# Kernel optimization log

Measured on AMD Instinct MI355X. Metric: run time of the kernel, lower is better.

The kernel has to match this reference:

```python
import jax, jax.numpy as jnp
import numpy as np

NUM_USERS = 100000
NUM_ITEMS = 50000
NUM_EDGES = 1000000
H = 64            # initial embedding dim
DIMS = [64, 64]   # per-layer output dims
B = 16384         # BPR batch size
NEG_SLOPE = 0.2
EPS = 1e-12


def setup_inputs() -> dict:
    key = jax.random.key(0)
    ks = jax.random.split(key, 20)
    s = 1.0 / np.sqrt(H)
    inp = {
        'user_emb': jax.random.normal(ks[0], (NUM_USERS, H), jnp.float32) * 0.1,
        'item_emb': jax.random.normal(ks[1], (NUM_ITEMS, H), jnp.float32) * 0.1,
        'W1_0': jax.random.normal(ks[2], (H, DIMS[0]), jnp.float32) * s,
        'b1_0': jnp.zeros((DIMS[0],), jnp.float32),
        'W2_0': jax.random.normal(ks[3], (H, DIMS[0]), jnp.float32) * s,
        'b2_0': jnp.zeros((DIMS[0],), jnp.float32),
        'W1_1': jax.random.normal(ks[4], (DIMS[0], DIMS[1]), jnp.float32) * s,
        'b1_1': jnp.zeros((DIMS[1],), jnp.float32),
        'W2_1': jax.random.normal(ks[5], (DIMS[0], DIMS[1]), jnp.float32) * s,
        'b2_1': jnp.zeros((DIMS[1],), jnp.float32),
        'edge_index': jnp.stack([
            jax.random.randint(ks[6], (NUM_EDGES,), 0, NUM_USERS),
            jax.random.randint(ks[7], (NUM_EDGES,), 0, NUM_ITEMS),
        ], axis=0),
        'users': jax.random.randint(ks[8], (B,), 0, NUM_USERS),
        'pos_items': jax.random.randint(ks[9], (B,), 0, NUM_ITEMS),
        'neg_items': jax.random.randint(ks[10], (B,), 0, NUM_ITEMS),
    }
    return inp


def _edge_norm(src, dst):
    # symmetric sqrt-degree norm: (deg_src * deg_dst) ** -0.5 per edge
    ones = jnp.ones(src.shape[0], jnp.float32)
    du = jax.ops.segment_sum(ones, src, num_segments=NUM_USERS)[src]
    di = jax.ops.segment_sum(ones, dst, num_segments=NUM_ITEMS)[dst]
    return ((du * di) ** -0.5)[:, None]  # [E, 1]


def _epilogue(h):
    # leaky_relu(0.2) -> (dropout eval = identity) -> L2 row-normalize
    h = jnp.where(h >= 0, h, NEG_SLOPE * h)
    n = jnp.sqrt(jnp.sum(h * h, axis=1, keepdims=True))
    return h / jnp.maximum(n, EPS)


def _layer(u, i, src, dst, norm, W1, b1, W2, b2):
    # node-level W1 transform, gathered per edge (same math as per-edge W1(x_j))
    u1 = u @ W1 + b1            # [Nu, d]
    i1 = i @ W1 + b1            # [Ni, d]
    cross = u[src] * i[dst]     # [E, din]  shared by both directions
    mW2 = cross @ W2 + b2       # [E, d]
    # user -> item: x_j = user[src], aggregate at item dst
    out_i = jax.ops.segment_sum(norm * u1[src] + mW2, dst, num_segments=NUM_ITEMS)
    # item -> user: x_j = item[dst], aggregate at user src
    out_u = jax.ops.segment_sum(norm * i1[dst] + mW2, src, num_segments=NUM_USERS)
    return _epilogue(out_u), _epilogue(out_i)


def reference(user_emb, item_emb, W1_0, b1_0, W2_0, b2_0, W1_1, b1_1, W2_1, b2_1,
              edge_index, users, pos_items, neg_items):
    src, dst = edge_index[0], edge_index[1]
    norm = _edge_norm(src, dst)
    u_list, i_list = [user_emb], [item_emb]
    u, i = user_emb, item_emb
    u, i = _layer(u, i, src, dst, norm, W1_0, b1_0, W2_0, b2_0)
    u_list.append(u); i_list.append(i)
    u, i = _layer(u, i, src, dst, norm, W1_1, b1_1, W2_1, b2_1)
    u_list.append(u); i_list.append(i)
    user_all = jnp.concatenate(u_list, axis=1)   # [Nu, H+sum(DIMS)]
    item_all = jnp.concatenate(i_list, axis=1)   # [Ni, H+sum(DIMS)]
    return (user_all[users], item_all[pos_items], item_all[neg_items])
```

## Files before the change

### kernel.cpp

```cpp
#include <hip/hip_runtime.h>

#define NU 100000
#define NI 50000
#define NE 1000000
#define NB 16384

#define UB ((NU + 1023) / 1024)
#define IB ((NI + 1023) / 1024)

#define NBKT_I ((NI + 127) >> 7)
#define NBKT_U ((NU + 255) >> 8)
#define EPB 2048

__global__ void deg_kernel(const int* __restrict__ ei, int* du, int* di) {
    int e = blockIdx.x * blockDim.x + threadIdx.x;
    if (e >= NE) return;
    atomicAdd(&du[ei[e]], 1);
    atomicAdd(&di[ei[NE + e]], 1);
}

__global__ __launch_bounds__(1024) void scan1_kernel(
        const int* __restrict__ du, const int* __restrict__ di,
        int* __restrict__ psum, float* __restrict__ rsd_u, float* __restrict__ rsd_i) {
    int b = blockIdx.x, tid = threadIdx.x;
    int v = 0;
    if (b < UB) {
        int i = b * 1024 + tid;
        if (i < NU) {
            int d = du[i]; v = d;
            rsd_u[i] = d > 0 ? 1.0f / sqrtf((float)d) : 0.f;
        }
    } else {
        int i = (b - UB) * 1024 + tid;
        if (i < NI) {
            int d = di[i]; v = d;
            rsd_i[i] = d > 0 ? 1.0f / sqrtf((float)d) : 0.f;
        }
    }
    int s = v;
    #pragma unroll
    for (int off = 32; off > 0; off >>= 1) s += __shfl_xor(s, off);
    __shared__ int ws[16];
    if ((tid & 63) == 0) ws[tid >> 6] = s;
    __syncthreads();
    if (tid == 0) {
        int t = 0;
        #pragma unroll
        for (int w = 0; w < 16; ++w) t += ws[w];
        psum[b] = t;
    }
}

__global__ __launch_bounds__(128) void scan2_kernel(int* __restrict__ psum) {
    int base = (blockIdx.x == 0) ? 0 : UB;
    int n = (blockIdx.x == 0) ? UB : IB;
    int tid = threadIdx.x;
    __shared__ int sh[128];
    int v = (tid < n) ? psum[base + tid] : 0;
    sh[tid] = v;
    __syncthreads();
    for (int off = 1; off < 128; off <<= 1) {
        int t = (tid >= off) ? sh[tid - off] : 0;
        __syncthreads();
        sh[tid] += t;
        __syncthreads();
    }
    if (tid < n) psum[base + tid] = sh[tid] - v;
}

__global__ __launch_bounds__(1024) void scan3_kernel(
        const int* __restrict__ du, const int* __restrict__ di,
        const int* __restrict__ psum,
        int* __restrict__ rp_u, int* __restrict__ rp_i,
        int* __restrict__ bcur_u, int* __restrict__ bcur_i) {
    int b = blockIdx.x, tid = threadIdx.x;
    bool isU = (b < UB);
    const int* deg = isU ? du : di;
    int* rp = isU ? rp_u : rp_i;
    int N = isU ? NU : NI;
    int i0 = isU ? b * 1024 : (b - UB) * 1024;
    int i = i0 + tid;
    int v = (i < N) ? deg[i] : 0;
    __shared__ int sh[1024];
    sh[tid] = v;
    __syncthreads();
    for (int off = 1; off < 1024; off <<= 1) {
        int t = (tid >= off) ? sh[tid - off] : 0;
        __syncthreads();
        sh[tid] += t;
        __syncthreads();
    }
    int excl = sh[tid] - v + psum[b];
    if (i < N) {
        rp[i] = excl;
        if (isU) { if ((i & 255) == 0) bcur_u[i >> 8] = excl; }
        else     { if ((i & 127) == 0) bcur_i[i >> 7] = excl; }
    }
    if (b == 0 && tid == 0) { rp_u[NU] = NE; rp_i[NI] = NE; }
}

__global__ __launch_bounds__(256) void binP1_kernel(
        const int* __restrict__ ei,
        int* __restrict__ bcur_i, int* __restrict__ bcur_u,
        int2* __restrict__ pairI, int2* __restrict__ pairU) {
    __shared__ int histA[NBKT_I], baseA[NBKT_I];
    __shared__ int histB[NBKT_U], baseB[NBKT_U];
    int t = threadIdx.x;
    int e0 = blockIdx.x * EPB;
    int cnt = min(EPB, NE - e0);
    int s[8], d[8];
    #pragma unroll
    for (int k = 0; k < 8; ++k) {
        int o = t + k * 256;
        if (o < cnt) { s[k] = ei[e0 + o]; d[k] = ei[NE + e0 + o]; }
        else { s[k] = -1; d[k] = -1; }
    }
    for (int x = t; x < NBKT_I; x += 256) histA[x] = 0;
    for (int x = t; x < NBKT_U; x += 256) histB[x] = 0;
    __syncthreads();
    #pragma unroll
    for (int k = 0; k < 8; ++k) {
        if (d[k] >= 0) {
            atomicAdd(&histA[d[k] >> 7], 1);
            atomicAdd(&histB[s[k] >> 8], 1);
        }
    }
    __syncthreads();
    for (int x = t; x < NBKT_I; x += 256) {
        int h = histA[x];
        baseA[x] = h ? atomicAdd(&bcur_i[x], h) : 0;
        histA[x] = 0;
    }
    for (int x = t; x < NBKT_U; x += 256) {
        int h = histB[x];
        baseB[x] = h ? atomicAdd(&bcur_u[x], h) : 0;
        histB[x] = 0;
    }
    __syncthreads();
    #pragma unroll
    for (int k = 0; k < 8; ++k) {
        if (d[k] >= 0) {
            int bI = d[k] >> 7;
            int off = atomicAdd(&histA[bI], 1);
            pairI[baseA[bI] + off] = make_int2(d[k], s[k]);
            int bU = s[k] >> 8;
            int off2 = atomicAdd(&histB[bU], 1);
            pairU[baseB[bU] + off2] = make_int2(s[k], d[k]);
        }
    }
}

__global__ __launch_bounds__(256) void binP2_kernel(
        const int2* __restrict__ pairI, const int2* __restrict__ pairU,
        const int* __restrict__ rp_i, const int* __restrict__ rp_u,
        const float* __restrict__ rsd_u, const float* __restrict__ rsd_i,
        int2* __restrict__ csr8_i, int2* __restrict__ csr8_u) {
    __shared__ int cur[256];
    int t = threadIdx.x;
    if (blockIdx.x < NBKT_I) {
        int b = blockIdx.x;
        int nb = b << 7, ne = min(nb + 128, NI);
        if (t < ne - nb) cur[t] = rp_i[nb + t];
        int wbeg = rp_i[nb], wend = rp_i[ne];
        __syncthreads();
        for (int j = wbeg + t; j < wend; j += 256) {
            int2 p = pairI[j];
            int slot = atomicAdd(&cur[p.x - nb], 1);
            csr8_i[slot] = make_int2(p.y, __float_as_int(rsd_u[p.y]));
        }
    } else {
        int b = blockIdx.x - NBKT_I;
        int nb = b << 8, ne = min(nb + 256, NU);
        if (t < ne - nb) cur[t] = rp_u[nb + t];
        int wbeg = rp_u[nb], wend = rp_u[ne];
        __syncthreads();
        for (int j = wbeg + t; j < wend; j += 256) {
            int2 p = pairU[j];
            int slot = atomicAdd(&cur[p.x - nb], 1);
            csr8_u[slot] = make_int2(p.y, __float_as_int(rsd_i[p.y]));
        }
    }
}

__global__ __launch_bounds__(256) void gatherA_kernel(
        const float* __restrict__ xu, const float* __restrict__ xi,
        const int* __restrict__ rp_u, const int* __restrict__ rp_i,
        const int2* __restrict__ csr8_u, const int2* __restrict__ csr8_i,
        const float* __restrict__ rsd_u, const float* __restrict__ rsd_i,
        float* __restrict__ acbuf_u, float* __restrict__ acbuf_i,
        float* __restrict__ swbuf_u, float* __restrict__ swbuf_i) {
    int n = (blockIdx.x * blockDim.x + threadIdx.x) >> 6;
    int lane = threadIdx.x & 63;
    if (n >= NI + NU) return;
    bool isItem = n < NI;
    int nn = isItem ? n : n - NI;
    const int* rp = isItem ? rp_i : rp_u;
    const int2* cs = isItem ? csr8_i : csr8_u;
    const float* x_own = isItem ? xi : xu;
    const float* emb_o = isItem ? xu : xi;
    float rs = isItem ? rsd_i[nn] : rsd_u[nn];
    float* acbuf = isItem ? acbuf_i : acbuf_u;
    float* swbuf = isItem ? swbuf_i : swbuf_u;

    int beg = rp[nn], end = rp[nn + 1];
    float sp = 0.f, ss = 0.f, swp = 0.f;
    for (int jj = beg; jj < end; jj += 64) {
        int m = min(64, end - jj);
        int2 rec = (lane < m) ? cs[jj + lane] : make_int2(0, 0);
        int idx = rec.x;
        float w = __int_as_float(rec.y);
        swp += w;
        int t = 0;
        for (; t + 3 < m; t += 4) {
            int s0 = __shfl(idx, t),     s1 = __shfl(idx, t + 1);
            int s2 = __shfl(idx, t + 2), s3 = __shfl(idx, t + 3);
            float w0 = __shfl(w, t),     w1 = __shfl(w, t + 1);
            float w2 = __shfl(w, t + 2), w3 = __shfl(w, t + 3);
            float v0 = emb_o[(size_t)s0 * 64 + lane];
            float v1 = emb_o[(size_t)s1 * 64 + lane];
            float v2 = emb_o[(size_t)s2 * 64 + lane];
            float v3 = emb_o[(size_t)s3 * 64 + lane];
            sp += (v0 + v1) + (v2 + v3);
            ss += w0 * v0 + w1 * v1 + w2 * v2 + w3 * v3;
        }
        for (; t < m; ++t) {
            int s0 = __shfl(idx, t);
            float w0 = __shfl(w, t);
            float v0 = emb_o[(size_t)s0 * 64 + lane];
            sp += v0; ss += w0 * v0;
        }
    }
    #pragma unroll
    for (int off = 32; off > 0; off >>= 1) swp += __shfl_xor(swp, off);
    acbuf[(size_t)nn * 128 + lane] = rs * ss;
    acbuf[(size_t)nn * 128 + 64 + lane] = x_own[(size_t)nn * 64 + lane] * sp;
    if (lane == 0) swbuf[nn] = rs * swp;
}

#define TB 4
__global__ __launch_bounds__(256) void transformB_kernel(
        int N, const float* __restrict__ acbuf, const float* __restrict__ swbuf,
        const int* __restrict__ rp,
        const float* __restrict__ W1, const float* __restrict__ b1,
        const float* __restrict__ W2, const float* __restrict__ b2,
        float* __restrict__ out) {
    __shared__ float w1s[4096];
    __shared__ float w2s[4096];
    __shared__ float acs[4][TB * 128];
    int tid = threadIdx.x;
    #pragma unroll
    for (int r = 0; r < 4; ++r) {
        *(float4*)&w1s[(r * 256 + tid) * 4] = *(const float4*)&W1[(r * 256 + tid) * 4];
        *(float4*)&w2s[(r * 256 + tid) * 4] = *(const float4*)&W2[(r * 256 + tid) * 4];
    }
    __syncthreads();
    int wv = tid >> 6, lane = tid & 63;
    int n0 = (blockIdx.x * 4 + wv) * TB;
    if (n0 >= N) return;
    float* slab = acs[wv];
    int half = lane >> 5;
    int off = (lane & 31) * 4;
    #pragma unroll
    for (int pr = 0; pr < 2; ++pr) {
        int j = pr * 2 + half;
        int n = n0 + j; if (n >= N) n = N - 1;
        *(float4*)&slab[j * 128 + off] = *(const float4*)&acbuf[(size_t)n * 128 + off];
    }
    float acc[TB] = {0.f, 0.f, 0.f, 0.f};
    #pragma unroll 4
    for (int kq = 0; kq < 16; ++kq) {
        float4 aq[TB], cq[TB];
        #pragma unroll
        for (int j = 0; j < TB; ++j) {
            aq[j] = *(const float4*)&slab[j * 128 + kq * 4];
            cq[j] = *(const float4*)&slab[j * 128 + 64 + kq * 4];
        }
        #pragma unroll
        for (int kk = 0; kk < 4; ++kk) {
            int k = kq * 4 + kk;
            float w1v = w1s[k * 64 + lane];
            float w2v = w2s[k * 64 + lane];
            #pragma unroll
            for (int j = 0; j < TB; ++j)
                acc[j] += (&aq[j].x)[kk] * w1v + (&cq[j].x)[kk] * w2v;
        }
    }
    float b1v = b1[lane], b2v = b2[lane];
    #pragma unroll
    for (int j = 0; j < TB; ++j) {
        int n = n0 + j;
        if (n >= N) break;
        float dgf = (float)(rp[n + 1] - rp[n]);
        float h = acc[j] + swbuf[n] * b1v + dgf * b2v;
        h = h >= 0.f ? h : 0.2f * h;
        float nsq = h * h;
        #pragma unroll
        for (int o = 32; o > 0; o >>= 1) nsq += __shfl_xor(nsq, o);
        float nrm = sqrtf(nsq);
        out[(size_t)n * 64 + lane] = h / fmaxf(nrm, 1e-12f);
    }
}

__global__ void gather_kernel(const float* __restrict__ ue, const float* __restrict__ u1,
                              const float* __restrict__ u2, const float* __restrict__ ie,
                              const float* __restrict__ i1, const float* __restrict__ i2,
                              const int* __restrict__ users, const int* __restrict__ pos,
                              const int* __restrict__ neg, float4* __restrict__ out) {
    int idx = blockIdx.x * blockDim.x + threadIdx.x;
    if (idx >= 3 * NB * 48) return;
    int which = idx / (NB * 48);
    int rem = idx - which * (NB * 48);
    int b = rem / 48, c4 = rem - b * 48;
    int seg = c4 >> 4, cc = (c4 & 15) << 2;
    int row;
    const float* srcarr;
    if (which == 0) {
        row = users[b];
        srcarr = (seg == 0) ? ue : (seg == 1 ? u1 : u2);
    } else {
        row = (which == 1) ? pos[b] : neg[b];
        srcarr = (seg == 0) ? ie : (seg == 1 ? i1 : i2);
    }
    out[idx] = *(const float4*)&srcarr[(size_t)row * 64 + cc];
}

extern "C" void kernel_launch(void* const* d_in, const int* in_sizes, int n_in,
                              void* d_out, int out_size, void* d_ws, size_t ws_size,
                              hipStream_t stream) {
    const float* user_emb = (const float*)d_in[0];
    const float* item_emb = (const float*)d_in[1];
    const float* W1_0 = (const float*)d_in[2];
    const float* b1_0 = (const float*)d_in[3];
    const float* W2_0 = (const float*)d_in[4];
    const float* b2_0 = (const float*)d_in[5];
    const float* W1_1 = (const float*)d_in[6];
    const float* b1_1 = (const float*)d_in[7];
    const float* W2_1 = (const float*)d_in[8];
    const float* b2_1 = (const float*)d_in[9];
    const int* ei = (const int*)d_in[10];
    const int* users = (const int*)d_in[11];
    const int* pos = (const int*)d_in[12];
    const int* neg = (const int*)d_in[13];

    char* p = (char*)d_ws;
    int* du = (int*)p;          p += NU * 4;
    int* di = (int*)p;          p += NI * 4;
    float* rsd_u = (float*)p;   p += NU * 4;
    float* rsd_i = (float*)p;   p += NI * 4;
    int* psum = (int*)p;        p += (UB + IB) * 4;
    int* rp_u = (int*)p;        p += (NU + 1) * 4;
    int* rp_i = (int*)p;        p += (NI + 1) * 4;
    int* bcur_i = (int*)p;      p += NBKT_I * 4;
    int* bcur_u = (int*)p;      p += NBKT_U * 4;
    int2* csr8_u = (int2*)p;    p += (size_t)NE * 8;
    int2* csr8_i = (int2*)p;    p += (size_t)NE * 8;
    float* u1 = (float*)p;      p += (size_t)NU * 64 * 4;
    float* u2 = (float*)p;      p += (size_t)NU * 64 * 4;
    float* i1 = (float*)p;      p += (size_t)NI * 64 * 4;
    float* i2 = (float*)p;      p += (size_t)NI * 64 * 4;
    float* acbuf_u = (float*)p; p += (size_t)NU * 128 * 4;
    float* swbuf_u = (float*)p; p += NU * 4;
    float* swbuf_i = (float*)p; p += NI * 4;
    float* acbuf_i = u2;
    int2* pairI = (int2*)acbuf_u;
    int2* pairU = (int2*)(acbuf_u + (size_t)NE * 2);

    hipMemsetAsync(du, 0, (size_t)(NU + NI) * sizeof(int), stream);

    deg_kernel<<<(NE + 255) / 256, 256, 0, stream>>>(ei, du, di);
    scan1_kernel<<<UB + IB, 1024, 0, stream>>>(du, di, psum, rsd_u, rsd_i);
    scan2_kernel<<<2, 128, 0, stream>>>(psum);
    scan3_kernel<<<UB + IB, 1024, 0, stream>>>(du, di, psum, rp_u, rp_i, bcur_u, bcur_i);
    binP1_kernel<<<(NE + EPB - 1) / EPB, 256, 0, stream>>>(ei, bcur_i, bcur_u, pairI, pairU);
    binP2_kernel<<<NBKT_I + NBKT_U, 256, 0, stream>>>(pairI, pairU, rp_i, rp_u,
                                                      rsd_u, rsd_i, csr8_i, csr8_u);

    const int GA = ((NI + NU) * 64 + 255) / 256;
    const int GB_I = (NI + 4 * TB - 1) / (4 * TB);
    const int GB_U = (NU + 4 * TB - 1) / (4 * TB);

    gatherA_kernel<<<GA, 256, 0, stream>>>(user_emb, item_emb, rp_u, rp_i, csr8_u, csr8_i,
                                           rsd_u, rsd_i, acbuf_u, acbuf_i, swbuf_u, swbuf_i);
    transformB_kernel<<<GB_I, 256, 0, stream>>>(NI, acbuf_i, swbuf_i, rp_i,
                                                W1_0, b1_0, W2_0, b2_0, i1);
    transformB_kernel<<<GB_U, 256, 0, stream>>>(NU, acbuf_u, swbuf_u, rp_u,
                                                W1_0, b1_0, W2_0, b2_0, u1);
    gatherA_kernel<<<GA, 256, 0, stream>>>(u1, i1, rp_u, rp_i, csr8_u, csr8_i,
                                           rsd_u, rsd_i, acbuf_u, acbuf_i, swbuf_u, swbuf_i);
    transformB_kernel<<<GB_I, 256, 0, stream>>>(NI, acbuf_i, swbuf_i, rp_i,
                                                W1_1, b1_1, W2_1, b2_1, i2);
    transformB_kernel<<<GB_U, 256, 0, stream>>>(NU, acbuf_u, swbuf_u, rp_u,
                                                W1_1, b1_1, W2_1, b2_1, u2);

    gather_kernel<<<(3 * NB * 48 + 255) / 256, 256, 0, stream>>>(
        user_emb, u1, u2, item_emb, i1, i2, users, pos, neg, (float4*)d_out);
}
```

Baseline: 656.2 us.

## Store gathered embeddings and intermediate accumulators in bf16 to halve gather traffic

A new kernel converts the input user and item embeddings to bf16 up front. Layer-0 transformB also writes a bf16 copy of its output, so the neighbour gathers in gatherA read 2-byte values instead of 4-byte ones. The gatherA-to-transformB accumulator buffer is also stored in bf16, with workspace regions re-aliased to hold these copies. The goal is to cut memory traffic in the bandwidth-bound random gathers, at the cost of an extra conversion pass, extra bf16 writes and reduced precision that may approach the accuracy tolerance.

```diff
diff --git a/kernel.cpp b/kernel.cpp
--- a/kernel.cpp
+++ b/kernel.cpp
@@ -11,12 +11,40 @@
 #define NBKT_I ((NI + 127) >> 7)
 #define NBKT_U ((NU + 255) >> 8)
 #define EPB 2048
+
+typedef unsigned short u16;
+typedef unsigned int u32;
+
+__device__ __forceinline__ u16 f2bf(float f) {
+    u32 u = __float_as_uint(f);
+    u32 r = u + 0x7FFFu + ((u >> 16) & 1u);
+    return (u16)(r >> 16);
+}
+__device__ __forceinline__ float bf2f(u16 s) {
+    return __uint_as_float(((u32)s) << 16);
+}
 
 __global__ void deg_kernel(const int* __restrict__ ei, int* du, int* di) {
     int e = blockIdx.x * blockDim.x + threadIdx.x;
     if (e >= NE) return;
     atomicAdd(&du[ei[e]], 1);
     atomicAdd(&di[ei[NE + e]], 1);
+}
+
+__global__ void convert_kernel(const float4* __restrict__ ue4, const float4* __restrict__ ie4,
+                               ushort4* __restrict__ ueb4, ushort4* __restrict__ ieb4) {
+    int i = blockIdx.x * blockDim.x + threadIdx.x;
+    const int TU = NU * 16;
+    if (i < TU) {
+        float4 v = ue4[i];
+        ushort4 r; r.x = f2bf(v.x); r.y = f2bf(v.y); r.z = f2bf(v.z); r.w = f2bf(v.w);
+        ueb4[i] = r;
+    } else if (i < TU + NI * 16) {
+        int j = i - TU;
+        float4 v = ie4[j];
+        ushort4 r; r.x = f2bf(v.x); r.y = f2bf(v.y); r.z = f2bf(v.z); r.w = f2bf(v.w);
+        ieb4[j] = r;
+    }
 }
 
 __global__ __launch_bounds__(1024) void scan1_kernel(
@@ -184,10 +212,11 @@
 
 __global__ __launch_bounds__(256) void gatherA_kernel(
         const float* __restrict__ xu, const float* __restrict__ xi,
+        const u16* __restrict__ ub, const u16* __restrict__ ib,
         const int* __restrict__ rp_u, const int* __restrict__ rp_i,
         const int2* __restrict__ csr8_u, const int2* __restrict__ csr8_i,
         const float* __restrict__ rsd_u, const float* __restrict__ rsd_i,
-        float* __restrict__ acbuf_u, float* __restrict__ acbuf_i,
+        u16* __restrict__ acbuf_u, u16* __restrict__ acbuf_i,
         float* __restrict__ swbuf_u, float* __restrict__ swbuf_i) {
     int n = (blockIdx.x * blockDim.x + threadIdx.x) >> 6;
     int lane = threadIdx.x & 63;
@@ -197,9 +226,9 @@
     const int* rp = isItem ? rp_i : rp_u;
     const int2* cs = isItem ? csr8_i : csr8_u;
     const float* x_own = isItem ? xi : xu;
-    const float* emb_o = isItem ? xu : xi;
+    const u16* emb_o = isItem ? ub : ib;
     float rs = isItem ? rsd_i[nn] : rsd_u[nn];
-    float* acbuf = isItem ? acbuf_i : acbuf_u;
+    u16* acbuf = isItem ? acbuf_i : acbuf_u;
     float* swbuf = isItem ? swbuf_i : swbuf_u;
 
     int beg = rp[nn], end = rp[nn + 1];
@@ -216,34 +245,34 @@
             int s2 = __shfl(idx, t + 2), s3 = __shfl(idx, t + 3);
             float w0 = __shfl(w, t),     w1 = __shfl(w, t + 1);
             float w2 = __shfl(w, t + 2), w3 = __shfl(w, t + 3);
-            float v0 = emb_o[(size_t)s0 * 64 + lane];
-            float v1 = emb_o[(size_t)s1 * 64 + lane];
-            float v2 = emb_o[(size_t)s2 * 64 + lane];
-            float v3 = emb_o[(size_t)s3 * 64 + lane];
+            float v0 = bf2f(emb_o[(size_t)s0 * 64 + lane]);
+            float v1 = bf2f(emb_o[(size_t)s1 * 64 + lane]);
+            float v2 = bf2f(emb_o[(size_t)s2 * 64 + lane]);
+            float v3 = bf2f(emb_o[(size_t)s3 * 64 + lane]);
             sp += (v0 + v1) + (v2 + v3);
             ss += w0 * v0 + w1 * v1 + w2 * v2 + w3 * v3;
         }
         for (; t < m; ++t) {
             int s0 = __shfl(idx, t);
             float w0 = __shfl(w, t);
-            float v0 = emb_o[(size_t)s0 * 64 + lane];
+            float v0 = bf2f(emb_o[(size_t)s0 * 64 + lane]);
             sp += v0; ss += w0 * v0;
         }
     }
     #pragma unroll
     for (int off = 32; off > 0; off >>= 1) swp += __shfl_xor(swp, off);
-    acbuf[(size_t)nn * 128 + lane] = rs * ss;
-    acbuf[(size_t)nn * 128 + 64 + lane] = x_own[(size_t)nn * 64 + lane] * sp;
+    acbuf[(size_t)nn * 128 + lane] = f2bf(rs * ss);
+    acbuf[(size_t)nn * 128 + 64 + lane] = f2bf(x_own[(size_t)nn * 64 + lane] * sp);
     if (lane == 0) swbuf[nn] = rs * swp;
 }
 
 #define TB 4
 __global__ __launch_bounds__(256) void transformB_kernel(
-        int N, const float* __restrict__ acbuf, const float* __restrict__ swbuf,
+        int N, const u16* __restrict__ acbuf, const float* __restrict__ swbuf,
         const int* __restrict__ rp,
         const float* __restrict__ W1, const float* __restrict__ b1,
         const float* __restrict__ W2, const float* __restrict__ b2,
-        float* __restrict__ out) {
+        float* __restrict__ out, u16* __restrict__ outb) {
     __shared__ float w1s[4096];
     __shared__ float w2s[4096];
     __shared__ float acs[4][TB * 128];
@@ -258,13 +287,13 @@
     int n0 = (blockIdx.x * 4 + wv) * TB;
     if (n0 >= N) return;
     float* slab = acs[wv];
-    int half = lane >> 5;
-    int off = (lane & 31) * 4;
-    #pragma unroll
-    for (int pr = 0; pr < 2; ++pr) {
-        int j = pr * 2 + half;
+    #pragma unroll
+    for (int j = 0; j < TB; ++j) {
         int n = n0 + j; if (n >= N) n = N - 1;
-        *(float4*)&slab[j * 128 + off] = *(const float4*)&acbuf[(size_t)n * 128 + off];
+        u32 u = *(const u32*)&acbuf[(size_t)n * 128 + lane * 2];
+        float2 f = make_float2(__uint_as_float(u << 16),
+                               __uint_as_float(u & 0xffff0000u));
+        *(float2*)&slab[j * 128 + lane * 2] = f;
     }
     float acc[TB] = {0.f, 0.f, 0.f, 0.f};
     #pragma unroll 4
@@ -296,8 +325,9 @@
         float nsq = h * h;
         #pragma unroll
         for (int o = 32; o > 0; o >>= 1) nsq += __shfl_xor(nsq, o);
-        float nrm = sqrtf(nsq);
-        out[(size_t)n * 64 + lane] = h / fmaxf(nrm, 1e-12f);
+        float res = h / fmaxf(sqrtf(nsq), 1e-12f);
+        out[(size_t)n * 64 + lane] = res;
+        if (outb) outb[(size_t)n * 64 + lane] = f2bf(res);
     }
 }
 
@@ -358,15 +388,21 @@
     float* u2 = (float*)p;      p += (size_t)NU * 64 * 4;
     float* i1 = (float*)p;      p += (size_t)NI * 64 * 4;
     float* i2 = (float*)p;      p += (size_t)NI * 64 * 4;
-    float* acbuf_u = (float*)p; p += (size_t)NU * 128 * 4;
+    u16* acbuf_u = (u16*)p;     p += (size_t)NU * 128 * 2;
     float* swbuf_u = (float*)p; p += NU * 4;
     float* swbuf_i = (float*)p; p += NI * 4;
-    float* acbuf_i = u2;
+    u16* u1b = (u16*)p;         p += (size_t)NU * 64 * 2;
+    u16* i1b = (u16*)p;         p += (size_t)NI * 64 * 2;
+    u16* acbuf_i = (u16*)u2;
+    u16* ueb = (u16*)((char*)u2 + (size_t)NU * 64 * 2);
+    u16* ieb = (u16*)i2;
     int2* pairI = (int2*)acbuf_u;
-    int2* pairU = (int2*)(acbuf_u + (size_t)NE * 2);
+    int2* pairU = pairI + NE;
 
     hipMemsetAsync(du, 0, (size_t)(NU + NI) * sizeof(int), stream);
 
+    convert_kernel<<<((NU + NI) * 16 + 255) / 256, 256, 0, stream>>>(
+        (const float4*)user_emb, (const float4*)item_emb, (ushort4*)ueb, (ushort4*)ieb);
     deg_kernel<<<(NE + 255) / 256, 256, 0, stream>>>(ei, du, di);
     scan1_kernel<<<UB + IB, 1024, 0, stream>>>(du, di, psum, rsd_u, rsd_i);
     scan2_kernel<<<2, 128, 0, stream>>>(psum);
@@ -379,18 +415,20 @@
     const int GB_I = (NI + 4 * TB - 1) / (4 * TB);
     const int GB_U = (NU + 4 * TB - 1) / (4 * TB);
 
-    gatherA_kernel<<<GA, 256, 0, stream>>>(user_emb, item_emb, rp_u, rp_i, csr8_u, csr8_i,
-                                           rsd_u, rsd_i, acbuf_u, acbuf_i, swbuf_u, swbuf_i);
+    gatherA_kernel<<<GA, 256, 0, stream>>>(user_emb, item_emb, ueb, ieb,
+                                           rp_u, rp_i, csr8_u, csr8_i, rsd_u, rsd_i,
+                                           acbuf_u, acbuf_i, swbuf_u, swbuf_i);
     transformB_kernel<<<GB_I, 256, 0, stream>>>(NI, acbuf_i, swbuf_i, rp_i,
-                                                W1_0, b1_0, W2_0, b2_0, i1);
+                                                W1_0, b1_0, W2_0, b2_0, i1, i1b);
     transformB_kernel<<<GB_U, 256, 0, stream>>>(NU, acbuf_u, swbuf_u, rp_u,
-                                                W1_0, b1_0, W2_0, b2_0, u1);
-    gatherA_kernel<<<GA, 256, 0, stream>>>(u1, i1, rp_u, rp_i, csr8_u, csr8_i,
-                                           rsd_u, rsd_i, acbuf_u, acbuf_i, swbuf_u, swbuf_i);
+                                                W1_0, b1_0, W2_0, b2_0, u1, u1b);
+    gatherA_kernel<<<GA, 256, 0, stream>>>(u1, i1, u1b, i1b,
+                                           rp_u, rp_i, csr8_u, csr8_i, rsd_u, rsd_i,
+                                           acbuf_u, acbuf_i, swbuf_u, swbuf_i);
     transformB_kernel<<<GB_I, 256, 0, stream>>>(NI, acbuf_i, swbuf_i, rp_i,
-                                                W1_1, b1_1, W2_1, b2_1, i2);
+                                                W1_1, b1_1, W2_1, b2_1, i2, (u16*)nullptr);
     transformB_kernel<<<GB_U, 256, 0, stream>>>(NU, acbuf_u, swbuf_u, rp_u,
-                                                W1_1, b1_1, W2_1, b2_1, u2);
+                                                W1_1, b1_1, W2_1, b2_1, u2, (u16*)nullptr);
 
     gather_kernel<<<(3 * NB * 48 + 255) / 256, 256, 0, stream>>>(
         user_emb, u1, u2, item_emb, i1, i2, users, pos, neg, (float4*)d_out);
```

Result: faster. 636.7 us (-3.0%).
